# Kernel optimization log

Hardware: AMD Instinct MI355X
Metric: run time of the kernel (lower is better)

## Reference

```python
import jax, jax.numpy as jnp
import numpy as np

N = 50000      # nodes
E = 800000     # edges (avg degree 16)
D_IN, D_H, D_OUT = 128, 128, 64


def setup_inputs() -> dict:
    key = jax.random.key(0)
    ks = jax.random.split(key, 12)
    s = 0.05  # weight init scale
    return {
        "x": jax.random.normal(ks[0], (N, D_IN), jnp.float32),
        "edge_index": jax.random.randint(ks[1], (2, E), 0, N, dtype=jnp.int64),
        "Wl0": jax.random.normal(ks[2], (D_H, D_IN), jnp.float32) * s,
        "bl0": jax.random.normal(ks[3], (D_H,), jnp.float32) * s,
        "Wr0": jax.random.normal(ks[4], (D_H, D_IN), jnp.float32) * s,
        "Wl1": jax.random.normal(ks[5], (D_H, D_H), jnp.float32) * s,
        "bl1": jax.random.normal(ks[6], (D_H,), jnp.float32) * s,
        "Wr1": jax.random.normal(ks[7], (D_H, D_H), jnp.float32) * s,
        "Wl2": jax.random.normal(ks[8], (D_OUT, D_H), jnp.float32) * s,
        "bl2": jax.random.normal(ks[9], (D_OUT,), jnp.float32) * s,
        "Wr2": jax.random.normal(ks[10], (D_OUT, D_H), jnp.float32) * s,
    }


def _sage_layer(h, src, dst, Wl, bl, Wr):
    # mean aggregation over incoming neighbors: out[i] = mean_{j in N(i)} h[j]
    n = h.shape[0]
    agg = jax.ops.segment_sum(h[src], dst, num_segments=n)          # [N, D]
    deg = jax.ops.segment_sum(jnp.ones((src.shape[0],), h.dtype), dst,
                              num_segments=n)                        # [N]
    mean = agg / jnp.maximum(deg, 1.0)[:, None]  # empty rows -> 0, matches torch_sparse
    # lin_l(agg) + lin_r(self); lin_r has no bias in PyG SAGEConv
    return mean @ Wl.T + bl + h @ Wr.T


def reference(x, edge_index, Wl0, bl0, Wr0, Wl1, bl1, Wr1, Wl2, bl2, Wr2):
    src, dst = edge_index[1], edge_index[0]  # adj row = dst, col = src
    h = jax.nn.relu(_sage_layer(x, src, dst, Wl0, bl0, Wr0))
    h = jax.nn.relu(_sage_layer(h, src, dst, Wl1, bl1, Wr1))
    h = _sage_layer(h, src, dst, Wl2, bl2, Wr2)
    return jax.nn.log_softmax(h, axis=1)
```

## Files before the change

kernel.cpp:

```cpp
#include <hip/hip_runtime.h>
#include <hip/hip_bf16.h>


typedef __attribute__((ext_vector_type(8))) short bf16x8;
typedef __attribute__((ext_vector_type(4))) float f32x4;

#define NPB 128
#define BCAP 2560
#define EPB 8192
#define EPT 32
#define CPAD 16

__device__ __forceinline__ unsigned short f2bf(float f) {
    unsigned int u = __builtin_bit_cast(unsigned int, f);
    u += 0x7fffu + ((u >> 16) & 1u);
    return (unsigned short)(u >> 16);
}
__device__ __forceinline__ float bf2f(unsigned int bits16) {
    return __builtin_bit_cast(float, bits16 << 16);
}


__global__ __launch_bounds__(256) void dist_cast_kernel(const int* __restrict__ dst,
                                                        const int* __restrict__ srcv,
                                                        int* __restrict__ gcnt,
                                                        unsigned int* __restrict__ staging,
                                                        int E, int NBc, int DB, int XB,
                                                        const float* __restrict__ x,
                                                        unsigned short* __restrict__ xbf,
                                                        const float* p0, const float* p1,
                                                        const float* p2, const float* p3,
                                                        const float* p4, const float* p5,
                                                        unsigned short* __restrict__ wbf) {
    __shared__ unsigned int stage[EPB];
    __shared__ int hist[400];
    __shared__ int lstart[400];
    __shared__ int gbase[400];
    __shared__ int scanbuf[256];
    int bid = blockIdx.x;
    int t = threadIdx.x;

    if (bid >= DB && bid < DB + XB) {
        int base = (bid - DB) * 256 + t;
        int stride = XB * 256;
        const float2* x2 = (const float2*)x;
        unsigned int* xo = (unsigned int*)xbf;
#pragma unroll
        for (int k = 0; k < 4; ++k) {
            int idx = base + k * stride;
            float2 v = x2[idx];
            xo[idx] = (unsigned int)f2bf(v.x) | ((unsigned int)f2bf(v.y) << 16);
        }
        return;
    }
    if (bid >= DB + XB) {
        int w = (bid - DB - XB) * 256 + t;
        if (w < 40960) {
            const float* src;
            int local;
            if      (w < 8192)  { src = p0; local = w; }
            else if (w < 16384) { src = p1; local = w - 8192; }
            else if (w < 24576) { src = p2; local = w - 16384; }
            else if (w < 32768) { src = p3; local = w - 24576; }
            else if (w < 36864) { src = p4; local = w - 32768; }
            else                { src = p5; local = w - 36864; }
            float2 v = ((const float2*)src)[local];
            unsigned int p = (unsigned int)f2bf(v.x) | ((unsigned int)f2bf(v.y) << 16);
            ((unsigned int*)wbf)[w] = p;
        }
        return;
    }

    int e0 = bid * EPB;
    unsigned int w[EPT];

    for (int b = t; b < NBc + 1; b += 256) hist[b] = 0;
    __syncthreads();

#pragma unroll
    for (int i = 0; i < EPT; ++i) {
        int e = e0 + i * 256 + t;
        unsigned int word = 0xFFFFFFFFu;
        if (e < E) word = ((unsigned int)dst[e] << 16) | (unsigned int)srcv[e];
        w[i] = word;
        int b = (int)(word >> 23); if (b > NBc) b = NBc;
        atomicAdd(&hist[b], 1);
    }
    __syncthreads();

    int b0 = 2 * t, b1 = 2 * t + 1;
    int h0 = (b0 <= NBc) ? hist[b0] : 0;
    int h1 = (b1 <= NBc) ? hist[b1] : 0;
    int pair = h0 + h1;
    scanbuf[t] = pair;
    __syncthreads();
    for (int off = 1; off < 256; off <<= 1) {
        int v = (t >= off) ? scanbuf[t - off] : 0;
        __syncthreads();
        scanbuf[t] += v;
        __syncthreads();
    }
    int excl = scanbuf[t] - pair;
    if (b0 <= NBc) lstart[b0] = excl;
    if (b1 <= NBc) lstart[b1] = excl + h0;
    __syncthreads();

    for (int b = t; b < NBc; b += 256) {
        int h = hist[b];
        gbase[b] = h ? atomicAdd(&gcnt[b * CPAD], h) : 0;
    }
    for (int b = t; b < NBc + 1; b += 256) hist[b] = lstart[b];
    __syncthreads();

#pragma unroll
    for (int i = 0; i < EPT; ++i) {
        unsigned int word = w[i];
        int b = (int)(word >> 23); if (b > NBc) b = NBc;
        int p = atomicAdd(&hist[b], 1);
        stage[p] = word;
    }
    __syncthreads();

    int total = lstart[NBc];
    for (int i = t; i < total; i += 256) {
        unsigned int word = stage[i];
        int b = (int)(word >> 23);
        int gpos = gbase[b] + (i - lstart[b]);
        staging[(size_t)b * BCAP + gpos] = word;
    }
}


template<int GY>
__device__ __forceinline__ void gemm_body(int mb, int y,
                                          const unsigned short* __restrict__ H,
                                          const unsigned short* __restrict__ Wl,
                                          const unsigned short* __restrict__ Wr,
                                          unsigned short* __restrict__ Cl,
                                          unsigned short* __restrict__ Cr, int N) {
    __shared__ unsigned short clds[4 * 32 * 68];
    const int halfY = GY >> 1;
    const int ldc = GY * 32;
    int wave = threadIdx.x >> 6;
    int lane = threadIdx.x & 63;
    int l15 = lane & 15, quad = lane >> 4;
    bool isL = y < halfY;
    const unsigned short* W = isL ? Wl : Wr;
    unsigned short* Cp = isL ? Cl : Cr;
    int yy = isL ? y : y - halfY;
    int wrow0 = yy * 64;
    int col0 = yy * 64;
    int m0 = mb * 128 + wave * 32;

    int r0 = m0 + l15;      if (r0 > N - 1) r0 = N - 1;
    int r1 = m0 + 16 + l15; if (r1 > N - 1) r1 = N - 1;
    const bf16x8* A0 = (const bf16x8*)(H + (size_t)r0 * 128);
    const bf16x8* A1 = (const bf16x8*)(H + (size_t)r1 * 128);

    f32x4 acc[2][4] = {};
#pragma unroll
    for (int ks = 0; ks < 4; ++ks) {
        int vidx = ks * 4 + quad;
        bf16x8 a0 = A0[vidx];
        bf16x8 a1 = A1[vidx];
#pragma unroll
        for (int j = 0; j < 4; ++j) {
            const bf16x8* B = (const bf16x8*)(W + (size_t)(wrow0 + j * 16 + l15) * 128);
            bf16x8 b = B[vidx];
            acc[0][j] = __builtin_amdgcn_mfma_f32_16x16x32_bf16(a0, b, acc[0][j], 0, 0, 0);
            acc[1][j] = __builtin_amdgcn_mfma_f32_16x16x32_bf16(a1, b, acc[1][j], 0, 0, 0);
        }
    }

    unsigned short* slice = clds + wave * (32 * 68);
#pragma unroll
    for (int i = 0; i < 2; ++i)
#pragma unroll
        for (int j = 0; j < 4; ++j)
#pragma unroll
            for (int r = 0; r < 4; ++r)
                slice[(i * 16 + quad * 4 + r) * 68 + j * 16 + l15] = f2bf(acc[i][j][r]);
    __syncthreads();

    int rlo = lane >> 3, j8 = lane & 7;
#pragma unroll
    for (int pass = 0; pass < 4; ++pass) {
        int row_local = pass * 8 + rlo;
        const unsigned short* p = slice + row_local * 68 + j8 * 8;
        unsigned long long lo = *(const unsigned long long*)(p);
        unsigned long long hi = *(const unsigned long long*)(p + 4);
        int row = m0 + row_local;
        if (row < N) {
            unsigned long long* q = (unsigned long long*)(Cp + (size_t)row * ldc + col0 + j8 * 8);
            q[0] = lo;
            q[1] = hi;
        }
    }
}


__global__ __launch_bounds__(256) void build_gemm_kernel(const unsigned int* __restrict__ staging,
                                                         const int* __restrict__ gcnt,
                                                         int* __restrict__ row_ptr,
                                                         int* __restrict__ adj, int N, int NBc,
                                                         int gemmRows,
                                                         const unsigned short* __restrict__ H,
                                                         const unsigned short* __restrict__ Wl,
                                                         const unsigned short* __restrict__ Wr,
                                                         unsigned short* __restrict__ Cl,
                                                         unsigned short* __restrict__ Cr) {
    __shared__ int hist[NPB];
    __shared__ int scn[NPB];
    __shared__ int wsum[4];
    int bid = blockIdx.x;
    int t = threadIdx.x;

    if (bid >= NBc) {
        int gid = bid - NBc;
        int mb = gid % gemmRows;
        int yy = gid / gemmRows;
        gemm_body<4>(mb, yy, H, Wl, Wr, Cl, Cr, N);
        return;
    }

    int b = bid;
    int n0 = b * NPB;
    int nb = N - n0; if (nb > NPB) nb = NPB;
    int ec = gcnt[b * CPAD];
    const unsigned int* st = staging + (size_t)b * BCAP;

    int a = 0;
    for (int j = t; j < b; j += 256) a += gcnt[j * CPAD];
#pragma unroll
    for (int off = 32; off; off >>= 1) a += __shfl_xor(a, off);
    if ((t & 63) == 0) wsum[t >> 6] = a;
    if (t < NPB) hist[t] = 0;
    __syncthreads();
    int bb = wsum[0] + wsum[1] + wsum[2] + wsum[3];

    for (int i = t; i < ec; i += 256)
        atomicAdd(&hist[(st[i] >> 16) & (NPB - 1)], 1);
    __syncthreads();

    int v = (t < NPB) ? hist[t] : 0;
    if (t < NPB) scn[t] = v;
    __syncthreads();
    for (int off = 1; off < NPB; off <<= 1) {
        int u = (t >= off && t < NPB) ? scn[t - off] : 0;
        __syncthreads();
        if (t < NPB) scn[t] += u;
        __syncthreads();
    }
    if (t < NPB) hist[t] = scn[t] - v;
    if (t < nb) row_ptr[n0 + t] = bb + (scn[t] - v);
    if (b == NBc - 1 && t == 0) row_ptr[N] = bb + ec;
    __syncthreads();

    for (int i = t; i < ec; i += 256) {
        unsigned int pk = st[i];
        int p = atomicAdd(&hist[(pk >> 16) & (NPB - 1)], 1);
        adj[bb + p] = (int)(pk & 0xffffu);
    }
}


template<int GY>
__global__ __launch_bounds__(256) void gemm_mfma_kernel(const unsigned short* __restrict__ H,
                                                        const unsigned short* __restrict__ Wl,
                                                        const unsigned short* __restrict__ Wr,
                                                        unsigned short* __restrict__ Cl,
                                                        unsigned short* __restrict__ Cr,
                                                        int N) {
    gemm_body<GY>(blockIdx.x, blockIdx.y, Wl ? H : H, Wl, Wr, Cl, Cr, N);
}


__global__ __launch_bounds__(256) void agg_relu_kernel(const unsigned short* __restrict__ Cl,
                                                       const unsigned short* __restrict__ Cr,
                                                       const int* __restrict__ row_ptr,
                                                       const int* __restrict__ adj,
                                                       const float* __restrict__ bias,
                                                       unsigned short* __restrict__ hout, int N) {
    int pr = (int)((blockIdx.x * blockDim.x + threadIdx.x) >> 6);
    int lane = threadIdx.x & 63;
    int nodeA = pr * 2;
    if (nodeA >= N) return;
    int nodeB = nodeA + 1;
    bool hasB = nodeB < N;
    int g = lane >> 4, c = lane & 15;
    int begA = row_ptr[nodeA], endA = row_ptr[nodeA + 1];
    int begB = hasB ? row_ptr[nodeB] : 0;
    int endB = hasB ? row_ptr[nodeB + 1] : 0;
    float pA[8] = {}, pB[8] = {};

    int cntA = endA - begA; if (cntA > 64) cntA = 64;
    int cntB = endB - begB; if (cntB > 64) cntB = 64;
    int idxA = (cntA > 0) ? adj[begA + (lane < cntA ? lane : cntA - 1)] : 0;
    int idxB = (cntB > 0) ? adj[begB + (lane < cntB ? lane : cntB - 1)] : 0;
    int c1A = cntA - 1, c1B = cntB - 1;
    int mx = cntA > cntB ? cntA : cntB;
    for (int i = 0; i < mx; i += 16) {
        bool doA = i < cntA, doB = i < cntB;
        bf16x8 vA[4], vB[4];
        float mA[4], mB[4];
        if (doA) {
#pragma unroll
            for (int s = 0; s < 4; ++s) {
                int tt = i + s * 4 + g;
                int src = __shfl(idxA, tt > c1A ? c1A : tt);
                mA[s] = tt < cntA ? 1.f : 0.f;
                vA[s] = ((const bf16x8*)(Cl + (size_t)src * 128))[c];
            }
        }
        if (doB) {
#pragma unroll
            for (int s = 0; s < 4; ++s) {
                int tt = i + s * 4 + g;
                int src = __shfl(idxB, tt > c1B ? c1B : tt);
                mB[s] = tt < cntB ? 1.f : 0.f;
                vB[s] = ((const bf16x8*)(Cl + (size_t)src * 128))[c];
            }
        }
        if (doA) {
#pragma unroll
            for (int s = 0; s < 4; ++s)
#pragma unroll
                for (int k = 0; k < 8; ++k)
                    pA[k] += mA[s] * bf2f((unsigned short)vA[s][k]);
        }
        if (doB) {
#pragma unroll
            for (int s = 0; s < 4; ++s)
#pragma unroll
                for (int k = 0; k < 8; ++k)
                    pB[k] += mB[s] * bf2f((unsigned short)vB[s][k]);
        }
    }
    for (int e = begA + 64; e < endA; e += 64) {
        int cnt = endA - e; if (cnt > 64) cnt = 64;
        int idx = adj[e + (lane < cnt ? lane : cnt - 1)];
        int c1 = cnt - 1;
        for (int i = 0; i < cnt; i += 16) {
#pragma unroll
            for (int s = 0; s < 4; ++s) {
                int tt = i + s * 4 + g;
                int src = __shfl(idx, tt > c1 ? c1 : tt);
                float m = tt < cnt ? 1.f : 0.f;
                bf16x8 v = ((const bf16x8*)(Cl + (size_t)src * 128))[c];
#pragma unroll
                for (int k = 0; k < 8; ++k)
                    pA[k] += m * bf2f((unsigned short)v[k]);
            }
        }
    }
    for (int e = begB + 64; e < endB; e += 64) {
        int cnt = endB - e; if (cnt > 64) cnt = 64;
        int idx = adj[e + (lane < cnt ? lane : cnt - 1)];
        int c1 = cnt - 1;
        for (int i = 0; i < cnt; i += 16) {
#pragma unroll
            for (int s = 0; s < 4; ++s) {
                int tt = i + s * 4 + g;
                int src = __shfl(idx, tt > c1 ? c1 : tt);
                float m = tt < cnt ? 1.f : 0.f;
                bf16x8 v = ((const bf16x8*)(Cl + (size_t)src * 128))[c];
#pragma unroll
                for (int k = 0; k < 8; ++k)
                    pB[k] += m * bf2f((unsigned short)v[k]);
            }
        }
    }

#pragma unroll
    for (int k = 0; k < 8; ++k) {
        pA[k] += __shfl_xor(pA[k], 16);
        pA[k] += __shfl_xor(pA[k], 32);
        pB[k] += __shfl_xor(pB[k], 16);
        pB[k] += __shfl_xor(pB[k], 32);
    }

    int degA = endA - begA, degB = endB - begB;
    float invA = 1.0f / (float)(degA > 1 ? degA : 1);
    float invB = 1.0f / (float)(degB > 1 ? degB : 1);
    bf16x8 svA = ((const bf16x8*)(Cr + (size_t)nodeA * 128))[c];
    bf16x8 svB = hasB ? ((const bf16x8*)(Cr + (size_t)nodeB * 128))[c] : svA;
    float4 b0 = ((const float4*)bias)[2 * c];
    float4 b1 = ((const float4*)bias)[2 * c + 1];
    float bb[8] = {b0.x, b0.y, b0.z, b0.w, b1.x, b1.y, b1.z, b1.w};
    bf16x8 oA, oB;
#pragma unroll
    for (int k = 0; k < 8; ++k) {
        oA[k] = (short)f2bf(fmaxf(pA[k] * invA + bb[k] + bf2f((unsigned short)svA[k]), 0.f));
        oB[k] = (short)f2bf(fmaxf(pB[k] * invB + bb[k] + bf2f((unsigned short)svB[k]), 0.f));
    }
    if (g == 0)
        ((bf16x8*)(hout + (size_t)nodeA * 128))[c] = oA;
    else if (g == 1 && hasB)
        ((bf16x8*)(hout + (size_t)nodeB * 128))[c] = oB;
}


__global__ __launch_bounds__(256) void final_kernel(const unsigned short* __restrict__ Cl2,
                                                    const unsigned short* __restrict__ Cr2,
                                                    const int* __restrict__ row_ptr,
                                                    const int* __restrict__ adj,
                                                    const float* __restrict__ bias,
                                                    float* __restrict__ out, int N) {
    int pr = (int)((blockIdx.x * blockDim.x + threadIdx.x) >> 6);
    int lane = threadIdx.x & 63;
    int nodeA = pr * 2;
    if (nodeA >= N) return;
    int nodeB = nodeA + 1;
    bool hasB = nodeB < N;
    int g = lane >> 3, c = lane & 7;
    int begA = row_ptr[nodeA], endA = row_ptr[nodeA + 1];
    int begB = hasB ? row_ptr[nodeB] : 0;
    int endB = hasB ? row_ptr[nodeB + 1] : 0;
    float pA[8] = {}, pB[8] = {};

    int cntA = endA - begA; if (cntA > 64) cntA = 64;
    int cntB = endB - begB; if (cntB > 64) cntB = 64;
    int idxA = (cntA > 0) ? adj[begA + (lane < cntA ? lane : cntA - 1)] : 0;
    int idxB = (cntB > 0) ? adj[begB + (lane < cntB ? lane : cntB - 1)] : 0;
    int c1A = cntA - 1, c1B = cntB - 1;
    int mx = cntA > cntB ? cntA : cntB;
    for (int i = 0; i < mx; i += 16) {
        bool doA = i < cntA, doB = i < cntB;
        bf16x8 vA[2], vB[2];
        float mA[2], mB[2];
        if (doA) {
#pragma unroll
            for (int s = 0; s < 2; ++s) {
                int tt = i + s * 8 + g;
                int src = __shfl(idxA, tt > c1A ? c1A : tt);
                mA[s] = tt < cntA ? 1.f : 0.f;
                vA[s] = ((const bf16x8*)(Cl2 + (size_t)src * 64))[c];
            }
        }
        if (doB) {
#pragma unroll
            for (int s = 0; s < 2; ++s) {
                int tt = i + s * 8 + g;
                int src = __shfl(idxB, tt > c1B ? c1B : tt);
                mB[s] = tt < cntB ? 1.f : 0.f;
                vB[s] = ((const bf16x8*)(Cl2 + (size_t)src * 64))[c];
            }
        }
        if (doA) {
#pragma unroll
            for (int s = 0; s < 2; ++s)
#pragma unroll
                for (int k = 0; k < 8; ++k)
                    pA[k] += mA[s] * bf2f((unsigned short)vA[s][k]);
        }
        if (doB) {
#pragma unroll
            for (int s = 0; s < 2; ++s)
#pragma unroll
                for (int k = 0; k < 8; ++k)
                    pB[k] += mB[s] * bf2f((unsigned short)vB[s][k]);
        }
    }
    for (int e = begA + 64; e < endA; e += 64) {
        int cnt = endA - e; if (cnt > 64) cnt = 64;
        int idx = adj[e + (lane < cnt ? lane : cnt - 1)];
        int c1 = cnt - 1;
        for (int i = 0; i < cnt; i += 16) {
#pragma unroll
            for (int s = 0; s < 2; ++s) {
                int tt = i + s * 8 + g;
                int src = __shfl(idx, tt > c1 ? c1 : tt);
                float m = tt < cnt ? 1.f : 0.f;
                bf16x8 v = ((const bf16x8*)(Cl2 + (size_t)src * 64))[c];
#pragma unroll
                for (int k = 0; k < 8; ++k)
                    pA[k] += m * bf2f((unsigned short)v[k]);
            }
        }
    }
    for (int e = begB + 64; e < endB; e += 64) {
        int cnt = endB - e; if (cnt > 64) cnt = 64;
        int idx = adj[e + (lane < cnt ? lane : cnt - 1)];
        int c1 = cnt - 1;
        for (int i = 0; i < cnt; i += 16) {
#pragma unroll
            for (int s = 0; s < 2; ++s) {
                int tt = i + s * 8 + g;
                int src = __shfl(idx, tt > c1 ? c1 : tt);
                float m = tt < cnt ? 1.f : 0.f;
                bf16x8 v = ((const bf16x8*)(Cl2 + (size_t)src * 64))[c];
#pragma unroll
                for (int k = 0; k < 8; ++k)
                    pB[k] += m * bf2f((unsigned short)v[k]);
            }
        }
    }

#pragma unroll
    for (int k = 0; k < 8; ++k) {
        pA[k] += __shfl_xor(pA[k], 8);
        pA[k] += __shfl_xor(pA[k], 16);
        pA[k] += __shfl_xor(pA[k], 32);
        pB[k] += __shfl_xor(pB[k], 8);
        pB[k] += __shfl_xor(pB[k], 16);
        pB[k] += __shfl_xor(pB[k], 32);
    }

    int degA = endA - begA, degB = endB - begB;
    float invA = 1.0f / (float)(degA > 1 ? degA : 1);
    float invB = 1.0f / (float)(degB > 1 ? degB : 1);
    bf16x8 svA = ((const bf16x8*)(Cr2 + (size_t)nodeA * 64))[c];
    bf16x8 svB = hasB ? ((const bf16x8*)(Cr2 + (size_t)nodeB * 64))[c] : svA;
    float4 b0 = ((const float4*)bias)[2 * c];
    float4 b1 = ((const float4*)bias)[2 * c + 1];
    float bb[8] = {b0.x, b0.y, b0.z, b0.w, b1.x, b1.y, b1.z, b1.w};
    float uA[8], uB[8];
#pragma unroll
    for (int k = 0; k < 8; ++k) {
        uA[k] = pA[k] * invA + bb[k] + bf2f((unsigned short)svA[k]);
        uB[k] = pB[k] * invB + bb[k] + bf2f((unsigned short)svB[k]);
    }

    float mA_ = uA[0], mB_ = uB[0];
#pragma unroll
    for (int k = 1; k < 8; ++k) { mA_ = fmaxf(mA_, uA[k]); mB_ = fmaxf(mB_, uB[k]); }
#pragma unroll
    for (int off = 1; off < 8; off <<= 1) {
        mA_ = fmaxf(mA_, __shfl_xor(mA_, off));
        mB_ = fmaxf(mB_, __shfl_xor(mB_, off));
    }
    float seA = 0.f, seB = 0.f;
#pragma unroll
    for (int k = 0; k < 8; ++k) { seA += __expf(uA[k] - mA_); seB += __expf(uB[k] - mB_); }
#pragma unroll
    for (int off = 1; off < 8; off <<= 1) {
        seA += __shfl_xor(seA, off);
        seB += __shfl_xor(seB, off);
    }
    float lsA = __logf(seA), lsB = __logf(seB);

    if (g == 0) {
        float4 o0 = {uA[0] - mA_ - lsA, uA[1] - mA_ - lsA, uA[2] - mA_ - lsA, uA[3] - mA_ - lsA};
        float4 o1 = {uA[4] - mA_ - lsA, uA[5] - mA_ - lsA, uA[6] - mA_ - lsA, uA[7] - mA_ - lsA};
        ((float4*)(out + (size_t)nodeA * 64))[2 * c] = o0;
        ((float4*)(out + (size_t)nodeA * 64))[2 * c + 1] = o1;
    } else if (g == 1 && hasB) {
        float4 o0 = {uB[0] - mB_ - lsB, uB[1] - mB_ - lsB, uB[2] - mB_ - lsB, uB[3] - mB_ - lsB};
        float4 o1 = {uB[4] - mB_ - lsB, uB[5] - mB_ - lsB, uB[6] - mB_ - lsB, uB[7] - mB_ - lsB};
        ((float4*)(out + (size_t)nodeB * 64))[2 * c] = o0;
        ((float4*)(out + (size_t)nodeB * 64))[2 * c + 1] = o1;
    }
}


extern "C" void kernel_launch(void* const* d_in, const int* in_sizes, int n_in,
                              void* d_out, int out_size, void* d_ws, size_t ws_size,
                              hipStream_t stream) {
    const float* x   = (const float*)d_in[0];
    const int*   ei  = (const int*)d_in[1];
    const float* Wl0 = (const float*)d_in[2];
    const float* bl0 = (const float*)d_in[3];
    const float* Wr0 = (const float*)d_in[4];
    const float* Wl1 = (const float*)d_in[5];
    const float* bl1 = (const float*)d_in[6];
    const float* Wr1 = (const float*)d_in[7];
    const float* Wl2 = (const float*)d_in[8];
    const float* bl2 = (const float*)d_in[9];
    const float* Wr2 = (const float*)d_in[10];
    float* out = (float*)d_out;

    const int N  = in_sizes[0] / 128;
    const int E  = in_sizes[1] / 2;
    const int NB = (N + NPB - 1) / NPB;

    char* ws = (char*)d_ws;
    auto alloc = [&](size_t bytes) {
        char* p = ws;
        ws += (bytes + 255) & ~(size_t)255;
        return p;
    };
    int*   row_ptr    = (int*)alloc((size_t)(N + 1) * 4);
    int*   adj        = (int*)alloc((size_t)E * 4);
    int*   gcnt      = (int*)alloc((size_t)NB * CPAD * 4);
    unsigned int* staging = (unsigned int*)alloc((size_t)NB * BCAP * 4);
    unsigned short* xbf = (unsigned short*)alloc((size_t)N * 128 * 2);
    unsigned short* wbf = (unsigned short*)alloc((size_t)81920 * 2);
    unsigned short* Cl  = (unsigned short*)alloc((size_t)N * 128 * 2);
    unsigned short* Cr  = (unsigned short*)alloc((size_t)N * 128 * 2);
    unsigned short* hA  = (unsigned short*)alloc((size_t)N * 128 * 2);
    unsigned short* hB  = (unsigned short*)alloc((size_t)N * 128 * 2);

    const int* dstp = ei;
    const int* srcp = ei + E;

    unsigned short* wl0 = wbf;
    unsigned short* wr0 = wbf + 16384;
    unsigned short* wl1 = wbf + 32768;
    unsigned short* wr1 = wbf + 49152;
    unsigned short* wl2 = wbf + 65536;
    unsigned short* wr2 = wbf + 73728;

    dim3 blk(256);
    int DB = (E + EPB - 1) / EPB;
    int XB = (N * 64) / (256 * 4);
    int gemmRows = (N + 127) / 128;
    int pairBlocks = (((N + 1) / 2) * 64 + 255) / 256;

    hipMemsetAsync(gcnt, 0, (size_t)NB * CPAD * 4, stream);
    dist_cast_kernel<<<DB + XB + 160, blk, 0, stream>>>(dstp, srcp, gcnt, staging, E, NB,
                                                        DB, XB, x, xbf,
                                                        Wl0, Wr0, Wl1, Wr1, Wl2, Wr2, wbf);
    build_gemm_kernel<<<NB + gemmRows * 4, blk, 0, stream>>>(staging, gcnt, row_ptr, adj,
                                                             N, NB, gemmRows, xbf, wl0, wr0,
                                                             Cl, Cr);
    agg_relu_kernel<<<pairBlocks, blk, 0, stream>>>(Cl, Cr, row_ptr, adj, bl0, hA, N);
    gemm_mfma_kernel<4><<<dim3(gemmRows, 4), blk, 0, stream>>>(hA, wl1, wr1, Cl, Cr, N);
    agg_relu_kernel<<<pairBlocks, blk, 0, stream>>>(Cl, Cr, row_ptr, adj, bl1, hB, N);
    gemm_mfma_kernel<2><<<dim3(gemmRows, 2), blk, 0, stream>>>(hB, wl2, wr2, Cl, Cr, N);
    final_kernel<<<pairBlocks, blk, 0, stream>>>(Cl, Cr, row_ptr, adj, bl2, out, N);
}
```

Measured before the change: 273.3 us.

## Fuse all GNN stages into one persistent cooperative kernel with grid barriers

```diff
diff --git a/kernel.cpp b/kernel.cpp
--- a/kernel.cpp
+++ b/kernel.cpp
@@ -7,8 +7,8 @@
 
 #define NPB 128
 #define BCAP 2560
-#define EPB 8192
-#define EPT 32
+#define EPB 4096
+#define EPT 16
 #define CPAD 16
 
 __device__ __forceinline__ unsigned short f2bf(float f) {
@@ -21,124 +21,37 @@
 }
 
 
-__global__ __launch_bounds__(256) void dist_cast_kernel(const int* __restrict__ dst,
-                                                        const int* __restrict__ srcv,
-                                                        int* __restrict__ gcnt,
-                                                        unsigned int* __restrict__ staging,
-                                                        int E, int NBc, int DB, int XB,
-                                                        const float* __restrict__ x,
-                                                        unsigned short* __restrict__ xbf,
-                                                        const float* p0, const float* p1,
-                                                        const float* p2, const float* p3,
-                                                        const float* p4, const float* p5,
-                                                        unsigned short* __restrict__ wbf) {
-    __shared__ unsigned int stage[EPB];
-    __shared__ int hist[400];
-    __shared__ int lstart[400];
-    __shared__ int gbase[400];
-    __shared__ int scanbuf[256];
-    int bid = blockIdx.x;
-    int t = threadIdx.x;
-
-    if (bid >= DB && bid < DB + XB) {
-        int base = (bid - DB) * 256 + t;
-        int stride = XB * 256;
-        const float2* x2 = (const float2*)x;
-        unsigned int* xo = (unsigned int*)xbf;
-#pragma unroll
-        for (int k = 0; k < 4; ++k) {
-            int idx = base + k * stride;
-            float2 v = x2[idx];
-            xo[idx] = (unsigned int)f2bf(v.x) | ((unsigned int)f2bf(v.y) << 16);
-        }
-        return;
-    }
-    if (bid >= DB + XB) {
-        int w = (bid - DB - XB) * 256 + t;
-        if (w < 40960) {
-            const float* src;
-            int local;
-            if      (w < 8192)  { src = p0; local = w; }
-            else if (w < 16384) { src = p1; local = w - 8192; }
-            else if (w < 24576) { src = p2; local = w - 16384; }
-            else if (w < 32768) { src = p3; local = w - 24576; }
-            else if (w < 36864) { src = p4; local = w - 32768; }
-            else                { src = p5; local = w - 36864; }
-            float2 v = ((const float2*)src)[local];
-            unsigned int p = (unsigned int)f2bf(v.x) | ((unsigned int)f2bf(v.y) << 16);
-            ((unsigned int*)wbf)[w] = p;
-        }
-        return;
-    }
-
-    int e0 = bid * EPB;
-    unsigned int w[EPT];
-
-    for (int b = t; b < NBc + 1; b += 256) hist[b] = 0;
+__device__ __forceinline__ void grid_barrier(unsigned* cnt, unsigned* gen, unsigned nb) {
     __syncthreads();
-
-#pragma unroll
-    for (int i = 0; i < EPT; ++i) {
-        int e = e0 + i * 256 + t;
-        unsigned int word = 0xFFFFFFFFu;
-        if (e < E) word = ((unsigned int)dst[e] << 16) | (unsigned int)srcv[e];
-        w[i] = word;
-        int b = (int)(word >> 23); if (b > NBc) b = NBc;
-        atomicAdd(&hist[b], 1);
+    if (threadIdx.x == 0) {
+        __threadfence();
+        unsigned g = __hip_atomic_load(gen, __ATOMIC_RELAXED, __HIP_MEMORY_SCOPE_AGENT);
+        unsigned old = __hip_atomic_fetch_add(cnt, 1u, __ATOMIC_ACQ_REL,
+                                              __HIP_MEMORY_SCOPE_AGENT);
+        if (old == nb - 1u) {
+            __hip_atomic_store(cnt, 0u, __ATOMIC_RELAXED, __HIP_MEMORY_SCOPE_AGENT);
+            __hip_atomic_fetch_add(gen, 1u, __ATOMIC_ACQ_REL, __HIP_MEMORY_SCOPE_AGENT);
+        } else {
+            int spin = 0;
+            while (__hip_atomic_load(gen, __ATOMIC_ACQUIRE, __HIP_MEMORY_SCOPE_AGENT) == g) {
+                __builtin_amdgcn_s_sleep(8);
+                if (++spin > 100000) break;
+            }
+        }
+        __threadfence();
     }
     __syncthreads();
-
-    int b0 = 2 * t, b1 = 2 * t + 1;
-    int h0 = (b0 <= NBc) ? hist[b0] : 0;
-    int h1 = (b1 <= NBc) ? hist[b1] : 0;
-    int pair = h0 + h1;
-    scanbuf[t] = pair;
-    __syncthreads();
-    for (int off = 1; off < 256; off <<= 1) {
-        int v = (t >= off) ? scanbuf[t - off] : 0;
-        __syncthreads();
-        scanbuf[t] += v;
-        __syncthreads();
-    }
-    int excl = scanbuf[t] - pair;
-    if (b0 <= NBc) lstart[b0] = excl;
-    if (b1 <= NBc) lstart[b1] = excl + h0;
-    __syncthreads();
-
-    for (int b = t; b < NBc; b += 256) {
-        int h = hist[b];
-        gbase[b] = h ? atomicAdd(&gcnt[b * CPAD], h) : 0;
-    }
-    for (int b = t; b < NBc + 1; b += 256) hist[b] = lstart[b];
-    __syncthreads();
-
-#pragma unroll
-    for (int i = 0; i < EPT; ++i) {
-        unsigned int word = w[i];
-        int b = (int)(word >> 23); if (b > NBc) b = NBc;
-        int p = atomicAdd(&hist[b], 1);
-        stage[p] = word;
-    }
-    __syncthreads();
-
-    int total = lstart[NBc];
-    for (int i = t; i < total; i += 256) {
-        unsigned int word = stage[i];
-        int b = (int)(word >> 23);
-        int gpos = gbase[b] + (i - lstart[b]);
-        staging[(size_t)b * BCAP + gpos] = word;
-    }
 }
 
 
 template<int GY>
-__device__ __forceinline__ void gemm_body(int mb, int y,
+__device__ __forceinline__ void gemm_body(unsigned char* smem, int mb, int y,
                                           const unsigned short* __restrict__ H,
                                           const unsigned short* __restrict__ Wl,
                                           const unsigned short* __restrict__ Wr,
                                           unsigned short* __restrict__ Cl,
                                           unsigned short* __restrict__ Cr, int N) {
-    __shared__ unsigned short clds[4 * 32 * 68];
+    unsigned short* clds = (unsigned short*)smem;
     const int halfY = GY >> 1;
     const int ldc = GY * 32;
     int wave = threadIdx.x >> 6;
@@ -196,93 +109,17 @@
             q[1] = hi;
         }
     }
-}
-
-
-__global__ __launch_bounds__(256) void build_gemm_kernel(const unsigned int* __restrict__ staging,
-                                                         const int* __restrict__ gcnt,
-                                                         int* __restrict__ row_ptr,
-                                                         int* __restrict__ adj, int N, int NBc,
-                                                         int gemmRows,
-                                                         const unsigned short* __restrict__ H,
-                                                         const unsigned short* __restrict__ Wl,
-                                                         const unsigned short* __restrict__ Wr,
-                                                         unsigned short* __restrict__ Cl,
-                                                         unsigned short* __restrict__ Cr) {
-    __shared__ int hist[NPB];
-    __shared__ int scn[NPB];
-    __shared__ int wsum[4];
-    int bid = blockIdx.x;
-    int t = threadIdx.x;
-
-    if (bid >= NBc) {
-        int gid = bid - NBc;
-        int mb = gid % gemmRows;
-        int yy = gid / gemmRows;
-        gemm_body<4>(mb, yy, H, Wl, Wr, Cl, Cr, N);
-        return;
-    }
-
-    int b = bid;
-    int n0 = b * NPB;
-    int nb = N - n0; if (nb > NPB) nb = NPB;
-    int ec = gcnt[b * CPAD];
-    const unsigned int* st = staging + (size_t)b * BCAP;
-
-    int a = 0;
-    for (int j = t; j < b; j += 256) a += gcnt[j * CPAD];
-#pragma unroll
-    for (int off = 32; off; off >>= 1) a += __shfl_xor(a, off);
-    if ((t & 63) == 0) wsum[t >> 6] = a;
-    if (t < NPB) hist[t] = 0;
     __syncthreads();
-    int bb = wsum[0] + wsum[1] + wsum[2] + wsum[3];
-
-    for (int i = t; i < ec; i += 256)
-        atomicAdd(&hist[(st[i] >> 16) & (NPB - 1)], 1);
-    __syncthreads();
-
-    int v = (t < NPB) ? hist[t] : 0;
-    if (t < NPB) scn[t] = v;
-    __syncthreads();
-    for (int off = 1; off < NPB; off <<= 1) {
-        int u = (t >= off && t < NPB) ? scn[t - off] : 0;
-        __syncthreads();
-        if (t < NPB) scn[t] += u;
-        __syncthreads();
-    }
-    if (t < NPB) hist[t] = scn[t] - v;
-    if (t < nb) row_ptr[n0 + t] = bb + (scn[t] - v);
-    if (b == NBc - 1 && t == 0) row_ptr[N] = bb + ec;
-    __syncthreads();
-
-    for (int i = t; i < ec; i += 256) {
-        unsigned int pk = st[i];
-        int p = atomicAdd(&hist[(pk >> 16) & (NPB - 1)], 1);
-        adj[bb + p] = (int)(pk & 0xffffu);
-    }
-}
-
-
-template<int GY>
-__global__ __launch_bounds__(256) void gemm_mfma_kernel(const unsigned short* __restrict__ H,
-                                                        const unsigned short* __restrict__ Wl,
-                                                        const unsigned short* __restrict__ Wr,
-                                                        unsigned short* __restrict__ Cl,
-                                                        unsigned short* __restrict__ Cr,
-                                                        int N) {
-    gemm_body<GY>(blockIdx.x, blockIdx.y, Wl ? H : H, Wl, Wr, Cl, Cr, N);
-}
-
-
-__global__ __launch_bounds__(256) void agg_relu_kernel(const unsigned short* __restrict__ Cl,
-                                                       const unsigned short* __restrict__ Cr,
-                                                       const int* __restrict__ row_ptr,
-                                                       const int* __restrict__ adj,
-                                                       const float* __restrict__ bias,
-                                                       unsigned short* __restrict__ hout, int N) {
-    int pr = (int)((blockIdx.x * blockDim.x + threadIdx.x) >> 6);
-    int lane = threadIdx.x & 63;
+}
+
+
+__device__ __forceinline__ void agg_pair(int pr, int lane,
+                                         const unsigned short* __restrict__ Cl,
+                                         const unsigned short* __restrict__ Cr,
+                                         const int* __restrict__ row_ptr,
+                                         const int* __restrict__ adj,
+                                         const float* __restrict__ bias,
+                                         unsigned short* __restrict__ hout, int N) {
     int nodeA = pr * 2;
     if (nodeA >= N) return;
     int nodeB = nodeA + 1;
@@ -400,14 +237,13 @@
 }
 
 
-__global__ __launch_bounds__(256) void final_kernel(const unsigned short* __restrict__ Cl2,
-                                                    const unsigned short* __restrict__ Cr2,
-                                                    const int* __restrict__ row_ptr,
-                                                    const int* __restrict__ adj,
-                                                    const float* __restrict__ bias,
-                                                    float* __restrict__ out, int N) {
-    int pr = (int)((blockIdx.x * blockDim.x + threadIdx.x) >> 6);
-    int lane = threadIdx.x & 63;
+__device__ __forceinline__ void final_pair(int pr, int lane,
+                                           const unsigned short* __restrict__ Cl2,
+                                           const unsigned short* __restrict__ Cr2,
+                                           const int* __restrict__ row_ptr,
+                                           const int* __restrict__ adj,
+                                           const float* __restrict__ bias,
+                                           float* __restrict__ out, int N) {
     int nodeA = pr * 2;
     if (nodeA >= N) return;
     int nodeB = nodeA + 1;
@@ -550,6 +386,203 @@
         ((float4*)(out + (size_t)nodeB * 64))[2 * c] = o0;
         ((float4*)(out + (size_t)nodeB * 64))[2 * c + 1] = o1;
     }
+}
+
+
+__global__ __launch_bounds__(256, 4) void mega_kernel(
+        const int* __restrict__ dstp, const int* __restrict__ srcp,
+        int* __restrict__ gcnt, unsigned* __restrict__ bar,
+        unsigned int* __restrict__ staging,
+        int E, int N, int NBc, int DB, int XB, int gemmRows, int pairVB,
+        const float* __restrict__ x, unsigned short* __restrict__ xbf,
+        const float* __restrict__ w0, const float* __restrict__ w1,
+        const float* __restrict__ w2, const float* __restrict__ w3,
+        const float* __restrict__ w4, const float* __restrict__ w5,
+        unsigned short* __restrict__ wbf,
+        int* __restrict__ row_ptr, int* __restrict__ adj,
+        const float* __restrict__ bl0, const float* __restrict__ bl1,
+        const float* __restrict__ bl2,
+        unsigned short* __restrict__ Cl, unsigned short* __restrict__ Cr,
+        unsigned short* __restrict__ hA, unsigned short* __restrict__ hB,
+        float* __restrict__ out) {
+    __shared__ __align__(16) unsigned char smem[22208];
+    int t = threadIdx.x;
+    unsigned* bcnt = bar;
+    unsigned* bgen = bar + 16;
+    unsigned nb = gridDim.x;
+
+    const unsigned short* wl0 = wbf;
+    const unsigned short* wr0 = wbf + 16384;
+    const unsigned short* wl1 = wbf + 32768;
+    const unsigned short* wr1 = wbf + 49152;
+    const unsigned short* wl2 = wbf + 65536;
+    const unsigned short* wr2 = wbf + 73728;
+
+    int P1 = DB + XB + 160;
+    for (int vb = blockIdx.x; vb < P1; vb += gridDim.x) {
+        if (vb < DB) {
+            unsigned int* stage = (unsigned int*)smem;
+            int* hist   = (int*)(smem + 16384);
+            int* lstart = (int*)(smem + 16384 + 1600);
+            int* gbase  = (int*)(smem + 16384 + 3200);
+            int* scanbuf= (int*)(smem + 16384 + 4800);
+            int e0 = vb * EPB;
+            unsigned int w[EPT];
+
+            for (int b = t; b < NBc + 1; b += 256) hist[b] = 0;
+            __syncthreads();
+#pragma unroll
+            for (int i = 0; i < EPT; ++i) {
+                int e = e0 + i * 256 + t;
+                unsigned int word = 0xFFFFFFFFu;
+                if (e < E) word = ((unsigned int)dstp[e] << 16) | (unsigned int)srcp[e];
+                w[i] = word;
+                int b = (int)(word >> 23); if (b > NBc) b = NBc;
+                atomicAdd(&hist[b], 1);
+            }
+            __syncthreads();
+
+            int b0 = 2 * t, b1 = 2 * t + 1;
+            int h0 = (b0 <= NBc) ? hist[b0] : 0;
+            int h1 = (b1 <= NBc) ? hist[b1] : 0;
+            int pair = h0 + h1;
+            scanbuf[t] = pair;
+            __syncthreads();
+            for (int off = 1; off < 256; off <<= 1) {
+                int v = (t >= off) ? scanbuf[t - off] : 0;
+                __syncthreads();
+                scanbuf[t] += v;
+                __syncthreads();
+            }
+            int excl = scanbuf[t] - pair;
+            if (b0 <= NBc) lstart[b0] = excl;
+            if (b1 <= NBc) lstart[b1] = excl + h0;
+            __syncthreads();
+
+            for (int b = t; b < NBc; b += 256) {
+                int h = hist[b];
+                gbase[b] = h ? atomicAdd(&gcnt[b * CPAD], h) : 0;
+            }
+            for (int b = t; b < NBc + 1; b += 256) hist[b] = lstart[b];
+            __syncthreads();
+
+#pragma unroll
+            for (int i = 0; i < EPT; ++i) {
+                unsigned int word = w[i];
+                int b = (int)(word >> 23); if (b > NBc) b = NBc;
+                int p = atomicAdd(&hist[b], 1);
+                stage[p] = word;
+            }
+            __syncthreads();
+
+            int total = lstart[NBc];
+            for (int i = t; i < total; i += 256) {
+                unsigned int word = stage[i];
+                int b = (int)(word >> 23);
+                int gpos = gbase[b] + (i - lstart[b]);
+                staging[(size_t)b * BCAP + gpos] = word;
+            }
+            __syncthreads();
+        } else if (vb < DB + XB) {
+            int base = (vb - DB) * 256 + t;
+            int stride = XB * 256;
+            const float2* x2 = (const float2*)x;
+            unsigned int* xo = (unsigned int*)xbf;
+#pragma unroll
+            for (int k = 0; k < 4; ++k) {
+                int idx = base + k * stride;
+                float2 v = x2[idx];
+                xo[idx] = (unsigned int)f2bf(v.x) | ((unsigned int)f2bf(v.y) << 16);
+            }
+        } else {
+            int w = (vb - DB - XB) * 256 + t;
+            if (w < 40960) {
+                const float* src;
+                int local;
+                if      (w < 8192)  { src = w0; local = w; }
+                else if (w < 16384) { src = w1; local = w - 8192; }
+                else if (w < 24576) { src = w2; local = w - 16384; }
+                else if (w < 32768) { src = w3; local = w - 24576; }
+                else if (w < 36864) { src = w4; local = w - 32768; }
+                else                { src = w5; local = w - 36864; }
+                float2 v = ((const float2*)src)[local];
+                unsigned int p = (unsigned int)f2bf(v.x) | ((unsigned int)f2bf(v.y) << 16);
+                ((unsigned int*)wbf)[w] = p;
+            }
+        }
+    }
+    grid_barrier(bcnt, bgen, nb);
+
+    int P2 = NBc + gemmRows * 4;
+    for (int vb = blockIdx.x; vb < P2; vb += gridDim.x) {
+        if (vb >= NBc) {
+            int gid = vb - NBc;
+            gemm_body<4>(smem, gid % gemmRows, gid / gemmRows, xbf, wl0, wr0, Cl, Cr, N);
+            continue;
+        }
+        int* hist = (int*)smem;
+        int* scn  = (int*)(smem + 512);
+        int* wsum = (int*)(smem + 1024);
+        int b = vb;
+        int n0 = b * NPB;
+        int nbn = N - n0; if (nbn > NPB) nbn = NPB;
+        int ec = gcnt[b * CPAD];
+        const unsigned int* st = staging + (size_t)b * BCAP;
+
+        int a = 0;
+        for (int j = t; j < b; j += 256) a += gcnt[j * CPAD];
+#pragma unroll
+        for (int off = 32; off; off >>= 1) a += __shfl_xor(a, off);
+        if ((t & 63) == 0) wsum[t >> 6] = a;
+        if (t < NPB) hist[t] = 0;
+        __syncthreads();
+        int bb = wsum[0] + wsum[1] + wsum[2] + wsum[3];
+
+        for (int i = t; i < ec; i += 256)
+            atomicAdd(&hist[(st[i] >> 16) & (NPB - 1)], 1);
+        __syncthreads();
+
+        int v = (t < NPB) ? hist[t] : 0;
+        if (t < NPB) scn[t] = v;
+        __syncthreads();
+        for (int off = 1; off < NPB; off <<= 1) {
+            int u = (t >= off && t < NPB) ? scn[t - off] : 0;
+            __syncthreads();
+            if (t < NPB) scn[t] += u;
+            __syncthreads();
+        }
+        if (t < NPB) hist[t] = scn[t] - v;
+        if (t < nbn) row_ptr[n0 + t] = bb + (scn[t] - v);
+        if (b == NBc - 1 && t == 0) row_ptr[N] = bb + ec;
+        __syncthreads();
+
+        for (int i = t; i < ec; i += 256) {
+            unsigned int pk = st[i];
+            int p = atomicAdd(&hist[(pk >> 16) & (NPB - 1)], 1);
+            adj[bb + p] = (int)(pk & 0xffffu);
+        }
+        __syncthreads();
+    }
+    grid_barrier(bcnt, bgen, nb);
+
+    for (int vb = blockIdx.x; vb < pairVB; vb += gridDim.x)
+        agg_pair(vb * 4 + (t >> 6), t & 63, Cl, Cr, row_ptr, adj, bl0, hA, N);
+    grid_barrier(bcnt, bgen, nb);
+
+    for (int vb = blockIdx.x; vb < gemmRows * 4; vb += gridDim.x)
+        gemm_body<4>(smem, vb % gemmRows, vb / gemmRows, hA, wl1, wr1, Cl, Cr, N);
+    grid_barrier(bcnt, bgen, nb);
+
+    for (int vb = blockIdx.x; vb < pairVB; vb += gridDim.x)
+        agg_pair(vb * 4 + (t >> 6), t & 63, Cl, Cr, row_ptr, adj, bl1, hB, N);
+    grid_barrier(bcnt, bgen, nb);
+
+    for (int vb = blockIdx.x; vb < gemmRows * 2; vb += gridDim.x)
+        gemm_body<2>(smem, vb % gemmRows, vb / gemmRows, hB, wl2, wr2, Cl, Cr, N);
+    grid_barrier(bcnt, bgen, nb);
+
+    for (int vb = blockIdx.x; vb < pairVB; vb += gridDim.x)
+        final_pair(vb * 4 + (t >> 6), t & 63, Cl, Cr, row_ptr, adj, bl2, out, N);
 }
 
 
@@ -581,7 +614,7 @@
     };
     int*   row_ptr    = (int*)alloc((size_t)(N + 1) * 4);
     int*   adj        = (int*)alloc((size_t)E * 4);
-    int*   gcnt      = (int*)alloc((size_t)NB * CPAD * 4);
+    int*   gcnt       = (int*)alloc((size_t)NB * CPAD * 4 + 128);
     unsigned int* staging = (unsigned int*)alloc((size_t)NB * BCAP * 4);
     unsigned short* xbf = (unsigned short*)alloc((size_t)N * 128 * 2);
     unsigned short* wbf = (unsigned short*)alloc((size_t)81920 * 2);
@@ -592,30 +625,44 @@
 
     const int* dstp = ei;
     const int* srcp = ei + E;
-
-    unsigned short* wl0 = wbf;
-    unsigned short* wr0 = wbf + 16384;
-    unsigned short* wl1 = wbf + 32768;
-    unsigned short* wr1 = wbf + 49152;
-    unsigned short* wl2 = wbf + 65536;
-    unsigned short* wr2 = wbf + 73728;
-
-    dim3 blk(256);
+    unsigned* bar = (unsigned*)(gcnt + NB * CPAD);
+
     int DB = (E + EPB - 1) / EPB;
     int XB = (N * 64) / (256 * 4);
     int gemmRows = (N + 127) / 128;
-    int pairBlocks = (((N + 1) / 2) * 64 + 255) / 256;
-
-    hipMemsetAsync(gcnt, 0, (size_t)NB * CPAD * 4, stream);
-    dist_cast_kernel<<<DB + XB + 160, blk, 0, stream>>>(dstp, srcp, gcnt, staging, E, NB,
-                                                        DB, XB, x, xbf,
-                                                        Wl0, Wr0, Wl1, Wr1, Wl2, Wr2, wbf);
-    build_gemm_kernel<<<NB + gemmRows * 4, blk, 0, stream>>>(staging, gcnt, row_ptr, adj,
-                                                             N, NB, gemmRows, xbf, wl0, wr0,
-                                                             Cl, Cr);
-    agg_relu_kernel<<<pairBlocks, blk, 0, stream>>>(Cl, Cr, row_ptr, adj, bl0, hA, N);
-    gemm_mfma_kernel<4><<<dim3(gemmRows, 4), blk, 0, stream>>>(hA, wl1, wr1, Cl, Cr, N);
-    agg_relu_kernel<<<pairBlocks, blk, 0, stream>>>(Cl, Cr, row_ptr, adj, bl1, hB, N);
-    gemm_mfma_kernel<2><<<dim3(gemmRows, 2), blk, 0, stream>>>(hB, wl2, wr2, Cl, Cr, N);
-    final_kernel<<<pairBlocks, blk, 0, stream>>>(Cl, Cr, row_ptr, adj, bl2, out, N);
-}
+    int pairVB = ((N + 1) / 2 + 3) / 4;
+
+    static int gridBlocks = 0;
+    if (gridBlocks == 0) {
+        int dev = 0;
+        hipGetDevice(&dev);
+        int numCU = 0;
+        hipDeviceGetAttribute(&numCU, hipDeviceAttributeMultiprocessorCount, dev);
+        if (numCU < 1) numCU = 256;
+        int occ = 0;
+        hipOccupancyMaxActiveBlocksPerMultiprocessor(&occ, mega_kernel, 256, 0);
+        if (occ < 1) occ = 1;
+        gridBlocks = occ * numCU;
+        if (gridBlocks > 2048) gridBlocks = 2048;
+    }
+
+    hipMemsetAsync(gcnt, 0, (size_t)NB * CPAD * 4 + 128, stream);
+
+    int E_ = E, N_ = N, NB_ = NB;
+    void* args[] = { &dstp, &srcp, &gcnt, &bar, &staging,
+                     &E_, &N_, &NB_, &DB, &XB, &gemmRows, &pairVB,
+                     &x, &xbf,
+                     &Wl0, &Wr0, &Wl1, &Wr1, &Wl2, &Wr2, &wbf,
+                     &row_ptr, &adj, &bl0, &bl1, &bl2,
+                     &Cl, &Cr, &hA, &hB, &out };
+    hipError_t err = hipLaunchCooperativeKernel(mega_kernel, dim3(gridBlocks), dim3(256),
+                                                args, 0, stream);
+    if (err != hipSuccess) {
+        mega_kernel<<<gridBlocks, 256, 0, stream>>>(dstp, srcp, gcnt, bar, staging,
+                                                    E_, N_, NB_, DB, XB, gemmRows, pairVB,
+                                                    x, xbf,
+                                                    Wl0, Wr0, Wl1, Wr1, Wl2, Wr2, wbf,
+                                                    row_ptr, adj, bl0, bl1, bl2,
+                                                    Cl, Cr, hA, hB, out);
+    }
+}
```

Result: slower. 717.1 us (+162.4%).
